# Kernel tuning notes

Measured on AMD Instinct MI355X. Metric: run time of the kernel, lower is better.

The kernel has to match this reference:

```python
import jax, jax.numpy as jnp
import numpy as np

N_NODES = 81920
N_EDGES = 1310720
NODES_PER_GRAPH = 320
N_GRAPHS = N_NODES // NODES_PER_GRAPH  # 256
IN_DIM = 64
HID = 64
OUT = 64


def setup_inputs() -> dict:
    key = jax.random.key(0)
    ks = jax.random.split(key, 16)
    x = jax.random.normal(ks[0], (N_NODES, IN_DIM), dtype=jnp.float32)
    edge_index = jax.random.randint(ks[1], (2, N_EDGES), 0, N_NODES, dtype=jnp.int32)
    # sorted graph-membership vector: 256 graphs of 320 nodes each
    batch = (jnp.arange(N_NODES, dtype=jnp.int32) // NODES_PER_GRAPH)
    std = 1.0  # module re-inits nn.Linear weights with N(0, 1)
    dims = [(IN_DIM, HID), (HID, HID), (HID, OUT)]
    params = {}
    for i, (di, do) in enumerate(dims):
        params[f"Wl{i}"] = std * jax.random.normal(ks[2 + 3 * i], (di, do), dtype=jnp.float32)
        params[f"bl{i}"] = jnp.zeros((do,), dtype=jnp.float32)
        params[f"Wr{i}"] = std * jax.random.normal(ks[3 + 3 * i], (di, do), dtype=jnp.float32)
    return dict(x=x, edge_index=edge_index, batch=batch, **params)


def _sage_conv(x, src, dst, Wl, bl, Wr):
    # PyG SAGEConv (aggr='mean', root_weight=True):
    #   out = lin_l(mean_{j in N(i)} x_j) + lin_r(x_i)
    msg = x[src]                                              # [E, d] gather
    agg = jax.ops.segment_sum(msg, dst, num_segments=N_NODES)  # [N, d] scatter-add
    cnt = jax.ops.segment_sum(jnp.ones((src.shape[0],), x.dtype), dst,
                              num_segments=N_NODES)
    agg = agg / jnp.maximum(cnt, 1.0)[:, None]                # mean aggregation
    return agg @ Wl + bl + x @ Wr


def reference(x, edge_index, batch, Wl0, bl0, Wr0, Wl1, bl1, Wr1, Wl2, bl2, Wr2):
    src, dst = edge_index[0], edge_index[1]
    layers = [(Wl0, bl0, Wr0), (Wl1, bl1, Wr1), (Wl2, bl2, Wr2)]
    h = x
    for i, (Wl, bl, Wr) in enumerate(layers):
        h = _sage_conv(h, src, dst, Wl, bl, Wr)
        if i < len(layers) - 1:
            h = jax.nn.relu(h)
            # F.dropout is identity in eval mode (training=False)
    # unbatch + take node 0 of every graph: first index where batch == g
    first_idx = jnp.searchsorted(batch, jnp.arange(N_GRAPHS, dtype=batch.dtype))
    return h[first_idx]  # [N_GRAPHS, OUT]
```

## Files before the change

### kernel.cpp

```cpp
#include <hip/hip_runtime.h>

#define N_NODES 81920
#define N_EDGES 1310720
#define NG 256
#define D 64
#define TM 64
#define SA 65
#define SB 33
#define SC 36
#define NB 320
#define NBLK 1280
#define BMW 2560
#define HCHUNK 4096
#define EPT 16
#define CAP0 1280
#define CAP1 256
#define CAP2 64

typedef __attribute__((ext_vector_type(2))) short sbf2;

__device__ __forceinline__ bool tb(const unsigned* bm, int i) {
    return (bm[i >> 5] >> (i & 31)) & 1u;
}
__device__ __forceinline__ unsigned bf16rne(float f) {
    unsigned u = __float_as_uint(f);
    return (u + 0x7fffu + ((u >> 16) & 1u)) >> 16;
}
__device__ __forceinline__ float bfl(unsigned u) { return __uint_as_float(u << 16); }
__device__ __forceinline__ float bfh(unsigned u) { return __uint_as_float(u & 0xffff0000u); }


__global__ __launch_bounds__(256) void init_ws(float4* __restrict__ aggb4,
                                               unsigned* __restrict__ bms,
                                               int* __restrict__ indeg,
                                               int* __restrict__ n01,
                                               int* __restrict__ cur0,
                                               int* __restrict__ curS,
                                               int* __restrict__ cur1,
                                               int* __restrict__ cur2,
                                               const float2* __restrict__ x2,
                                               unsigned* __restrict__ xb) {
    int t = blockIdx.x * 256 + threadIdx.x;
    float4 z = make_float4(0.f, 0.f, 0.f, 0.f);
    aggb4[t] = z;
    aggb4[t + NBLK * 256] = z;
    if (t < 3 * BMW) bms[t] = 0u;
    if (t < N_NODES) indeg[t] = 0;
    if (t < 2) n01[t] = 0;
    if (t < NBLK) {
        cur0[t] = t * CAP0;
        curS[t] = t * CAP0;
        cur1[t] = t * CAP1;
        cur2[t] = t * CAP2;
    }
    #pragma unroll
    for (int i = 0; i < 8; ++i) {
        int idx = i * (NBLK * 256) + t;
        float2 v = x2[idx];
        xb[idx] = bf16rne(v.x) | (bf16rne(v.y) << 16);
    }
}


__global__ void ff_mark(const int* __restrict__ batch, int* __restrict__ fidx,
                        unsigned* __restrict__ bm2, unsigned* __restrict__ bm1,
                        float* __restrict__ aggf) {
    int i = blockIdx.x * 256 + threadIdx.x;
    int b = batch[i];
    if (i == 0 || batch[i - 1] != b) {
        fidx[b] = i;
        unsigned bit = 1u << (i & 31);
        atomicOr(&bm2[i >> 5], bit);
        atomicOr(&bm1[i >> 5], bit);
        float4* r = (float4*)&aggf[i * D];
        #pragma unroll
        for (int j = 0; j < 16; ++j) r[j] = make_float4(0.f, 0.f, 0.f, 0.f);
    }
}

__global__ void mark_srcs_bm(const int* __restrict__ src, const int* __restrict__ dst,
                             const unsigned* __restrict__ bmD, unsigned* __restrict__ bmS,
                             const unsigned* __restrict__ orsrc) {
    if (orsrc && blockIdx.x == 0) {
        for (int w = threadIdx.x; w < BMW; w += 256)
            if (orsrc[w]) atomicOr(&bmS[w], orsrc[w]);
    }
    int e = blockIdx.x * 256 + threadIdx.x;
    if (e < N_EDGES && tb(bmD, dst[e])) {
        int s = src[e];
        atomicOr(&bmS[s >> 5], 1u << (s & 31));
    }
}


__global__ __launch_bounds__(256) void build_staged(
    const int* __restrict__ src, const int* __restrict__ dst,
    const unsigned* __restrict__ bm0, const unsigned* __restrict__ bm1,
    const unsigned* __restrict__ bm2,
    int* __restrict__ cur0, int* __restrict__ curS,
    int* __restrict__ cur1, int* __restrict__ cur2,
    int* __restrict__ esp0, int* __restrict__ espS,
    int* __restrict__ esp1, int* __restrict__ esp2,
    int* __restrict__ list1, int* __restrict__ n1)
{
    __shared__ int hd[NBLK];
    __shared__ int hs[NBLK];
    __shared__ int bd[NBLK];
    __shared__ int bs[NBLK];
    const int tid = threadIdx.x;
    const int e0  = blockIdx.x * HCHUNK;

    for (int i = tid; i < NBLK; i += 256) { hd[i] = 0; hs[i] = 0; }

    {
        int i = blockIdx.x * 256 + tid;
        int lane = tid & 63;
        bool p1 = tb(bm1, i);
        unsigned long long b1 = __ballot(p1);
        int lt = __popcll(b1 & ((1ull << lane) - 1));
        int base = 0;
        if (lane == 0 && b1) base = atomicAdd(n1, __popcll(b1));
        base = __shfl(base, 0);
        if (p1) list1[base + lt] = i;
    }
    __syncthreads();

    int pk_r[EPT];
    int md_r[EPT];
    int ms_r[EPT];

    #pragma unroll
    for (int j = 0; j < EPT; ++j) {
        int e = e0 + j * 256 + tid;
        int d = dst[e];
        md_r[j] = -1;
        if (tb(bm0, d)) {
            int s  = src[e];
            int db = d >> 6;
            int sb = s >> 6;
            pk_r[j] = (s << 6) | (d & 63);
            md_r[j] = db | (atomicAdd(&hd[db], 1) << 11);
            ms_r[j] = sb | (atomicAdd(&hs[sb], 1) << 11);
            if (tb(bm1, d)) {
                int pk = (d << 6) | (s & 63);
                int p1 = atomicAdd(&cur1[sb], 1);
                if (p1 < sb * CAP1 + CAP1) esp1[p1] = pk;
                if (tb(bm2, d)) {
                    int p2 = atomicAdd(&cur2[sb], 1);
                    if (p2 < sb * CAP2 + CAP2) esp2[p2] = pk;
                }
            }
        }
    }
    __syncthreads();

    for (int i = tid; i < NBLK; i += 256) {
        int cd = hd[i];
        bd[i] = cd ? atomicAdd(&cur0[i], cd) : 0;
        int cs = hs[i];
        bs[i] = cs ? atomicAdd(&curS[i], cs) : 0;
    }
    __syncthreads();

    #pragma unroll
    for (int j = 0; j < EPT; ++j) {
        int md = md_r[j];
        if (md >= 0) {
            int db = md & 2047;
            int sb = ms_r[j] & 2047;
            int posd = bd[db] + (md >> 11);
            int poss = bs[sb] + (ms_r[j] >> 11);
            if (posd < db * CAP0 + CAP0 && poss < sb * CAP0 + CAP0) {
                esp0[posd] = pk_r[j];
                espS[poss] = (posd << 6) | ((pk_r[j] >> 6) & 63);
            }
        }
    }
}


__global__ __launch_bounds__(256) void build_push(const int* __restrict__ src,
                                                  const int* __restrict__ dst,
                                                  const unsigned* __restrict__ bm0,
                                                  const unsigned* __restrict__ bm1,
                                                  const unsigned* __restrict__ bm2,
                                                  int* __restrict__ cur0,
                                                  int* __restrict__ cur1,
                                                  int* __restrict__ cur2,
                                                  int* __restrict__ esp0,
                                                  int* __restrict__ esp1,
                                                  int* __restrict__ esp2,
                                                  int* __restrict__ indeg,
                                                  int* __restrict__ list1,
                                                  int* __restrict__ n1) {
    __shared__ int h0[NBLK];
    __shared__ int b0[NBLK];
    const int tid = threadIdx.x;
    const int e0  = blockIdx.x * HCHUNK;

    for (int i = tid; i < NBLK; i += 256) h0[i] = 0;

    {
        int i = blockIdx.x * 256 + tid;
        int lane = tid & 63;
        bool p1 = tb(bm1, i);
        unsigned long long b1 = __ballot(p1);
        int lt = __popcll(b1 & ((1ull << lane) - 1));
        int base = 0;
        if (lane == 0 && b1) base = atomicAdd(n1, __popcll(b1));
        base = __shfl(base, 0);
        if (p1) list1[base + lt] = i;
    }
    __syncthreads();

    int pk_r[EPT];
    int sb_r[EPT];
    int rk_r[EPT];

    #pragma unroll
    for (int j = 0; j < EPT; ++j) {
        int e = e0 + j * 256 + tid;
        int d = dst[e];
        sb_r[j] = -1;
        if (tb(bm0, d)) {
            int s  = src[e];
            int sb = s >> 6;
            int pk = (d << 6) | (s & 63);
            pk_r[j] = pk;
            sb_r[j] = sb;
            rk_r[j] = atomicAdd(&h0[sb], 1);
            atomicAdd(&indeg[d], 1);
            if (tb(bm1, d)) {
                int p1 = atomicAdd(&cur1[sb], 1);
                if (p1 < sb * CAP1 + CAP1) esp1[p1] = pk;
                if (tb(bm2, d)) {
                    int p2 = atomicAdd(&cur2[sb], 1);
                    if (p2 < sb * CAP2 + CAP2) esp2[p2] = pk;
                }
            }
        }
    }
    __syncthreads();

    for (int i = tid; i < NBLK; i += 256) {
        int c = h0[i];
        b0[i] = c ? atomicAdd(&cur0[i], c) : 0;
    }
    __syncthreads();

    #pragma unroll
    for (int j = 0; j < EPT; ++j) {
        int sb = sb_r[j];
        if (sb >= 0) {
            int pos = b0[sb] + rk_r[j];
            if (pos < sb * CAP0 + CAP0) esp0[pos] = pk_r[j];
        }
    }
}


__global__ __launch_bounds__(256, 8) void sage_stage_l0(
    const unsigned* __restrict__ xb, const int* __restrict__ curS,
    const int* __restrict__ espS, uint4* __restrict__ stage)
{
    __shared__ unsigned Rs[TM * SC];

    const int tid  = threadIdx.x;
    const int base = blockIdx.x * TM;
    const int lane = tid & 63;
    const int w    = tid >> 6;
    const int g    = lane >> 3;
    const int l3   = lane & 7;

    const int e0 = blockIdx.x * CAP0;
    const int e1 = min(curS[blockIdx.x], e0 + CAP0);
    if (e0 == e1) return;

    for (int idx = tid; idx < TM * 32; idx += 256) {
        int m = idx >> 5, k = idx & 31;
        Rs[m * SC + k] = xb[(base << 5) + idx];
    }
    __syncthreads();

    const int chunk = ((e1 - e0) + 3) >> 2;
    int e = e0 + w * chunk;
    const int ee = min(e + chunk, e1);

    for (; e + 64 <= ee; e += 64) {
        int pv = espS[e + lane];
        #pragma unroll
        for (int u = 0; u < 8; ++u) {
            int p = __shfl(pv, (u << 3) + g);
            uint4 v = *(const uint4*)&Rs[(p & 63) * SC + (l3 << 2)];
            stage[((p >> 6) << 3) + l3] = v;
        }
    }
    for (; e < ee; ++e) {
        int p = espS[e];
        if (lane < 8) {
            uint4 v = *(const uint4*)&Rs[(p & 63) * SC + (lane << 2)];
            stage[((p >> 6) << 3) + lane] = v;
        }
    }
}


__global__ __launch_bounds__(256, 4) void sage_reduce_l0(
    const unsigned* __restrict__ xb, const int* __restrict__ cur0,
    const int* __restrict__ esp0, const uint4* __restrict__ stage,
    int* __restrict__ indeg, float* __restrict__ hout,
    const float* __restrict__ Wl, const float* __restrict__ bl,
    const float* __restrict__ Wr)
{
    __shared__ float As[TM * SA];
    __shared__ float Xs[TM * SA];
    __shared__ float invs[TM];

    const int tid  = threadIdx.x;
    const int base = blockIdx.x * TM;
    const int lane = tid & 63;
    const int w    = tid >> 6;
    const int g    = lane >> 3;
    const int l3   = lane & 7;

    for (int idx = tid; idx < TM * SA; idx += 256) As[idx] = 0.f;
    for (int idx = tid; idx < TM * 32; idx += 256) {
        int m = idx >> 5, k2 = (idx & 31) << 1;
        unsigned xw = xb[(base << 5) + idx];
        Xs[m * SA + k2]     = bfl(xw);
        Xs[m * SA + k2 + 1] = bfh(xw);
    }
    __syncthreads();

    const int e0 = blockIdx.x * CAP0;
    const int e1 = min(cur0[blockIdx.x], e0 + CAP0);

    const int chunk = ((e1 - e0) + 3) >> 2;
    int e = e0 + w * chunk;
    const int ee = min(e + chunk, e1);

    for (; e + 64 <= ee; e += 64) {
        int pv = esp0[e + lane];
        #pragma unroll
        for (int u = 0; u < 8; ++u) {
            int ei = (u << 3) + g;
            int p  = __shfl(pv, ei);
            uint4 v = stage[((e + ei) << 3) + l3];
            int dl = p & 63;
            float* row = &As[dl * SA + (l3 << 3)];
            atomicAdd(&row[0], bfl(v.x));
            atomicAdd(&row[1], bfh(v.x));
            atomicAdd(&row[2], bfl(v.y));
            atomicAdd(&row[3], bfh(v.y));
            atomicAdd(&row[4], bfl(v.z));
            atomicAdd(&row[5], bfh(v.z));
            atomicAdd(&row[6], bfl(v.w));
            atomicAdd(&row[7], bfh(v.w));
            if (l3 == 0) atomicAdd(&As[dl * SA + 64], 1.0f);
        }
    }
    for (; e < ee; ++e) {
        int p = esp0[e];
        if (lane < 8) {
            uint4 v = stage[(e << 3) + lane];
            int dl = p & 63;
            float* row = &As[dl * SA + (lane << 3)];
            atomicAdd(&row[0], bfl(v.x));
            atomicAdd(&row[1], bfh(v.x));
            atomicAdd(&row[2], bfl(v.y));
            atomicAdd(&row[3], bfh(v.y));
            atomicAdd(&row[4], bfl(v.z));
            atomicAdd(&row[5], bfh(v.z));
            atomicAdd(&row[6], bfl(v.w));
            atomicAdd(&row[7], bfh(v.w));
            if (lane == 0) atomicAdd(&As[dl * SA + 64], 1.0f);
        }
    }
    __syncthreads();

    if (tid < TM) {
        int cn = (int)As[tid * SA + 64];
        indeg[base + tid] = cn;
        invs[tid] = 1.0f / (float)max(cn, 1);
    }
    __syncthreads();

    const int j0 = (tid & 7) << 3;
    const int m2 = (tid >> 3) << 1;
    const float iv0 = invs[m2];
    const float iv1 = invs[m2 + 1];
    float o[2][8];
    {
        float4 ba = *(const float4*)&bl[j0];
        float4 bb = *(const float4*)&bl[j0 + 4];
        #pragma unroll
        for (int mi = 0; mi < 2; ++mi) {
            o[mi][0] = ba.x; o[mi][1] = ba.y; o[mi][2] = ba.z; o[mi][3] = ba.w;
            o[mi][4] = bb.x; o[mi][5] = bb.y; o[mi][6] = bb.z; o[mi][7] = bb.w;
        }
    }
    #pragma unroll 8
    for (int k = 0; k < D; ++k) {
        float a0 = As[m2 * SA + k] * iv0;
        float a1 = As[(m2 + 1) * SA + k] * iv1;
        float x0 = Xs[m2 * SA + k];
        float x1 = Xs[(m2 + 1) * SA + k];
        float4 wl0 = *(const float4*)&Wl[(k << 6) + j0];
        float4 wl1 = *(const float4*)&Wl[(k << 6) + j0 + 4];
        float4 wr0 = *(const float4*)&Wr[(k << 6) + j0];
        float4 wr1 = *(const float4*)&Wr[(k << 6) + j0 + 4];
        o[0][0] += a0 * wl0.x + x0 * wr0.x;  o[1][0] += a1 * wl0.x + x1 * wr0.x;
        o[0][1] += a0 * wl0.y + x0 * wr0.y;  o[1][1] += a1 * wl0.y + x1 * wr0.y;
        o[0][2] += a0 * wl0.z + x0 * wr0.z;  o[1][2] += a1 * wl0.z + x1 * wr0.z;
        o[0][3] += a0 * wl0.w + x0 * wr0.w;  o[1][3] += a1 * wl0.w + x1 * wr0.w;
        o[0][4] += a0 * wl1.x + x0 * wr1.x;  o[1][4] += a1 * wl1.x + x1 * wr1.x;
        o[0][5] += a0 * wl1.y + x0 * wr1.y;  o[1][5] += a1 * wl1.y + x1 * wr1.y;
        o[0][6] += a0 * wl1.z + x0 * wr1.z;  o[1][6] += a1 * wl1.z + x1 * wr1.z;
        o[0][7] += a0 * wl1.w + x0 * wr1.w;  o[1][7] += a1 * wl1.w + x1 * wr1.w;
    }
    #pragma unroll
    for (int mi = 0; mi < 2; ++mi) {
        float4 r0 = make_float4(fmaxf(o[mi][0], 0.f), fmaxf(o[mi][1], 0.f),
                                fmaxf(o[mi][2], 0.f), fmaxf(o[mi][3], 0.f));
        float4 r1 = make_float4(fmaxf(o[mi][4], 0.f), fmaxf(o[mi][5], 0.f),
                                fmaxf(o[mi][6], 0.f), fmaxf(o[mi][7], 0.f));
        *(float4*)&hout[(base + m2 + mi) * D + j0]     = r0;
        *(float4*)&hout[(base + m2 + mi) * D + j0 + 4] = r1;
    }
}


__global__ __launch_bounds__(256, 8) void sage_push_bf_pre(
    const unsigned* __restrict__ xb, const int* __restrict__ cur,
    const int* __restrict__ esp, unsigned* __restrict__ aggb, int cap)
{
    __shared__ unsigned Rs[TM * SB];

    const int tid  = threadIdx.x;
    const int base = blockIdx.x * TM;
    const int lane = tid & 63;
    const int w    = tid >> 6;
    const int l5   = lane & 31;
    const int hi   = lane >> 5;

    const int e0 = blockIdx.x * cap;
    const int e1 = min(cur[blockIdx.x], e0 + cap);
    if (e0 == e1) return;

    for (int idx = tid; idx < TM * 32; idx += 256) {
        int m = idx >> 5, k = idx & 31;
        Rs[m * SB + k] = xb[(base << 5) + idx];
    }
    __syncthreads();

    const int chunk = ((e1 - e0) + 3) >> 2;
    int e = e0 + w * chunk;
    const int ee = min(e + chunk, e1);

    for (; e + 64 <= ee; e += 64) {
        int pv = esp[e + lane];
        #pragma unroll
        for (int u = 0; u < 32; ++u) {
            int p = __shfl(pv, (u << 1) + hi);
            unsigned v = Rs[(p & 63) * SB + l5];
            __builtin_amdgcn_global_atomic_fadd_v2bf16(
                (sbf2*)&aggb[((p >> 6) << 5) + l5], *(sbf2*)&v);
        }
    }
    for (; e < ee; ++e) {
        int p = esp[e];
        if (!hi) {
            unsigned v = Rs[(p & 63) * SB + l5];
            __builtin_amdgcn_global_atomic_fadd_v2bf16(
                (sbf2*)&aggb[((p >> 6) << 5) + l5], *(sbf2*)&v);
        }
    }
}


__global__ __launch_bounds__(256, 8) void sage_push_bf(
    const float* __restrict__ hin, const int* __restrict__ cur,
    const int* __restrict__ esp, unsigned* __restrict__ aggb, int cap)
{
    __shared__ unsigned Rs[TM * SB];

    const int tid  = threadIdx.x;
    const int base = blockIdx.x * TM;
    const int lane = tid & 63;
    const int w    = tid >> 6;
    const int l5   = lane & 31;
    const int hi   = lane >> 5;

    const int e0 = blockIdx.x * cap;
    const int e1 = min(cur[blockIdx.x], e0 + cap);
    if (e0 == e1) return;

    for (int idx = tid; idx < TM * 32; idx += 256) {
        int m = idx >> 5, k = idx & 31;
        float2 v = *(const float2*)&hin[((base + m) << 6) + (k << 1)];
        Rs[m * SB + k] = bf16rne(v.x) | (bf16rne(v.y) << 16);
    }
    __syncthreads();

    const int chunk = ((e1 - e0) + 3) >> 2;
    int e = e0 + w * chunk;
    const int ee = min(e + chunk, e1);

    for (; e + 64 <= ee; e += 64) {
        int pv = esp[e + lane];
        #pragma unroll
        for (int u = 0; u < 32; ++u) {
            int p = __shfl(pv, (u << 1) + hi);
            unsigned v = Rs[(p & 63) * SB + l5];
            __builtin_amdgcn_global_atomic_fadd_v2bf16(
                (sbf2*)&aggb[((p >> 6) << 5) + l5], *(sbf2*)&v);
        }
    }
    for (; e < ee; ++e) {
        int p = esp[e];
        if (!hi) {
            unsigned v = Rs[(p & 63) * SB + l5];
            __builtin_amdgcn_global_atomic_fadd_v2bf16(
                (sbf2*)&aggb[((p >> 6) << 5) + l5], *(sbf2*)&v);
        }
    }
}


__global__ __launch_bounds__(256, 8) void sage_push_f32(
    const float* __restrict__ hin, const int* __restrict__ cur,
    const int* __restrict__ esp, float* __restrict__ agg, int cap)
{
    __shared__ float Rs[TM * SA];

    const int tid  = threadIdx.x;
    const int base = blockIdx.x * TM;
    const int lane = tid & 63;
    const int w    = tid >> 6;

    const int e0 = blockIdx.x * cap;
    const int e1 = min(cur[blockIdx.x], e0 + cap);
    if (e0 == e1) return;

    for (int idx = tid; idx < TM * D; idx += 256) {
        int m = idx >> 6, k = idx & 63;
        Rs[m * SA + k] = hin[(base << 6) + idx];
    }
    __syncthreads();

    const int chunk = ((e1 - e0) + 3) >> 2;
    int e = e0 + w * chunk;
    const int ee = min(e + chunk, e1);

    for (; e < ee; ++e) {
        int p = esp[e];
        atomicAdd(&agg[(p & 0x7fffffc0) + lane], Rs[(p & 63) * SA + lane]);
    }
}


__global__ __launch_bounds__(256, 4) void sage_finish_dense(
    const unsigned* __restrict__ xb, unsigned* __restrict__ aggb,
    const int* __restrict__ indeg, float* __restrict__ hout,
    const float* __restrict__ Wl, const float* __restrict__ bl,
    const float* __restrict__ Wr)
{
    __shared__ float As[TM * SA];
    __shared__ float Xs[TM * SA];
    __shared__ float invs[TM];

    const int tid  = threadIdx.x;
    const int base = blockIdx.x * TM;

    if (tid < TM) invs[tid] = 1.0f / (float)max(indeg[base + tid], 1);
    for (int idx = tid; idx < TM * 32; idx += 256) {
        int m = idx >> 5, k2 = (idx & 31) << 1;
        unsigned v = aggb[(base << 5) + idx];
        As[m * SA + k2]     = bfl(v);
        As[m * SA + k2 + 1] = bfh(v);
        aggb[(base << 5) + idx] = 0u;
        unsigned xw = xb[(base << 5) + idx];
        Xs[m * SA + k2]     = bfl(xw);
        Xs[m * SA + k2 + 1] = bfh(xw);
    }
    __syncthreads();
    for (int idx = tid; idx < TM * D; idx += 256) {
        int m = idx >> 6, k = idx & 63;
        As[m * SA + k] *= invs[m];
    }
    __syncthreads();

    const int j0 = (tid & 15) << 2;
    const int m0 = (tid >> 4) << 2;
    float o[4][4];
    float4 b4 = *(const float4*)&bl[j0];
    #pragma unroll
    for (int mi = 0; mi < 4; ++mi) {
        o[mi][0] = b4.x; o[mi][1] = b4.y; o[mi][2] = b4.z; o[mi][3] = b4.w;
    }
    #pragma unroll 8
    for (int k = 0; k < D; ++k) {
        float4 wl = *(const float4*)&Wl[(k << 6) + j0];
        float4 wr = *(const float4*)&Wr[(k << 6) + j0];
        #pragma unroll
        for (int mi = 0; mi < 4; ++mi) {
            float a = As[(m0 + mi) * SA + k];
            float x = Xs[(m0 + mi) * SA + k];
            o[mi][0] += a * wl.x + x * wr.x;
            o[mi][1] += a * wl.y + x * wr.y;
            o[mi][2] += a * wl.z + x * wr.z;
            o[mi][3] += a * wl.w + x * wr.w;
        }
    }
    #pragma unroll
    for (int mi = 0; mi < 4; ++mi) {
        float4 r = make_float4(fmaxf(o[mi][0], 0.f), fmaxf(o[mi][1], 0.f),
                               fmaxf(o[mi][2], 0.f), fmaxf(o[mi][3], 0.f));
        *(float4*)&hout[(base + m0 + mi) * D + j0] = r;
    }
}


__global__ __launch_bounds__(256, 4) void sage_finish_sel(
    const float* __restrict__ hin, unsigned* __restrict__ aggb,
    const int* __restrict__ indeg, const int* __restrict__ list,
    const int* __restrict__ pcount, float* __restrict__ hout,
    const float* __restrict__ Wl, const float* __restrict__ bl,
    const float* __restrict__ Wr)
{
    __shared__ float As[TM * SA];
    __shared__ float Xs[TM * SA];
    __shared__ float invs[TM];
    __shared__ int   nid[TM];

    const int cntv = *pcount;
    const int base = blockIdx.x * TM;
    if (base >= cntv) return;

    const int tid = threadIdx.x;
    if (tid < TM) {
        int n = (base + tid < cntv) ? list[base + tid] : -1;
        nid[tid]  = n;
        invs[tid] = (n >= 0) ? 1.0f / (float)max(indeg[n], 1) : 0.f;
    }
    __syncthreads();
    for (int idx = tid; idx < TM * 32; idx += 256) {
        int m = idx >> 5, k2 = idx & 31;
        int n = nid[m];
        if (n >= 0) {
            unsigned v = aggb[(n << 5) + k2];
            As[m * SA + (k2 << 1)]     = bfl(v) * invs[m];
            As[m * SA + (k2 << 1) + 1] = bfh(v) * invs[m];
        } else {
            As[m * SA + (k2 << 1)]     = 0.f;
            As[m * SA + (k2 << 1) + 1] = 0.f;
        }
    }
    for (int idx = tid; idx < TM * D; idx += 256) {
        int m = idx >> 6, k = idx & 63;
        int n = nid[m];
        Xs[m * SA + k] = (n >= 0) ? hin[n * D + k] : 0.f;
    }
    __syncthreads();

    const int j0 = (tid & 15) << 2;
    const int m0 = (tid >> 4) << 2;
    float o[4][4];
    float4 b4 = *(const float4*)&bl[j0];
    #pragma unroll
    for (int mi = 0; mi < 4; ++mi) {
        o[mi][0] = b4.x; o[mi][1] = b4.y; o[mi][2] = b4.z; o[mi][3] = b4.w;
    }
    #pragma unroll 8
    for (int k = 0; k < D; ++k) {
        float4 wl = *(const float4*)&Wl[(k << 6) + j0];
        float4 wr = *(const float4*)&Wr[(k << 6) + j0];
        #pragma unroll
        for (int mi = 0; mi < 4; ++mi) {
            float a = As[(m0 + mi) * SA + k];
            float x = Xs[(m0 + mi) * SA + k];
            o[mi][0] += a * wl.x + x * wr.x;
            o[mi][1] += a * wl.y + x * wr.y;
            o[mi][2] += a * wl.z + x * wr.z;
            o[mi][3] += a * wl.w + x * wr.w;
        }
    }
    #pragma unroll
    for (int mi = 0; mi < 4; ++mi) {
        int n = nid[m0 + mi];
        if (n >= 0) {
            float4 r = make_float4(fmaxf(o[mi][0], 0.f), fmaxf(o[mi][1], 0.f),
                                   fmaxf(o[mi][2], 0.f), fmaxf(o[mi][3], 0.f));
            *(float4*)&hout[n * D + j0] = r;
        }
    }
}


__global__ __launch_bounds__(256, 3) void final_gemm_sel(
    const float* __restrict__ hin, const float* __restrict__ agg,
    const int* __restrict__ indeg, const int* __restrict__ fidx,
    const float* __restrict__ Wl, const float* __restrict__ bl,
    const float* __restrict__ Wr, float* __restrict__ out)
{
    __shared__ float As[TM * SA];
    __shared__ float Xs[TM * SA];
    __shared__ int   nid[TM];
    __shared__ float invs[TM];

    const int tid  = threadIdx.x;
    const int base = blockIdx.x * TM;

    if (tid < TM) {
        int n = fidx[base + tid];
        nid[tid]  = n;
        invs[tid] = 1.0f / (float)max(indeg[n], 1);
    }
    __syncthreads();
    for (int idx = tid; idx < TM * D; idx += 256) {
        int m = idx >> 6, k = idx & 63;
        int n = nid[m];
        As[m * SA + k] = agg[n * D + k] * invs[m];
        Xs[m * SA + k] = hin[n * D + k];
    }
    __syncthreads();

    const int j0 = (tid & 15) << 2;
    const int m0 = (tid >> 4) << 2;
    float o[4][4];
    float4 b4 = *(const float4*)&bl[j0];
    #pragma unroll
    for (int mi = 0; mi < 4; ++mi) {
        o[mi][0] = b4.x; o[mi][1] = b4.y; o[mi][2] = b4.z; o[mi][3] = b4.w;
    }
    #pragma unroll 8
    for (int k = 0; k < D; ++k) {
        float4 wl = *(const float4*)&Wl[(k << 6) + j0];
        float4 wr = *(const float4*)&Wr[(k << 6) + j0];
        #pragma unroll
        for (int mi = 0; mi < 4; ++mi) {
            float a = As[(m0 + mi) * SA + k];
            float x = Xs[(m0 + mi) * SA + k];
            o[mi][0] += a * wl.x + x * wr.x;
            o[mi][1] += a * wl.y + x * wr.y;
            o[mi][2] += a * wl.z + x * wr.z;
            o[mi][3] += a * wl.w + x * wr.w;
        }
    }
    #pragma unroll
    for (int mi = 0; mi < 4; ++mi) {
        float4 r = make_float4(o[mi][0], o[mi][1], o[mi][2], o[mi][3]);
        *(float4*)&out[(base + m0 + mi) * D + j0] = r;
    }
}


extern "C" void kernel_launch(void* const* d_in, const int* in_sizes, int n_in,
                              void* d_out, int out_size, void* d_ws, size_t ws_size,
                              hipStream_t stream)
{
    const float* x     = (const float*)d_in[0];
    const int*   ei    = (const int*)d_in[1];
    const int*   batch = (const int*)d_in[2];
    const float* Wl0 = (const float*)d_in[3];
    const float* bl0 = (const float*)d_in[4];
    const float* Wr0 = (const float*)d_in[5];
    const float* Wl1 = (const float*)d_in[6];
    const float* bl1 = (const float*)d_in[7];
    const float* Wr1 = (const float*)d_in[8];
    const float* Wl2 = (const float*)d_in[9];
    const float* bl2 = (const float*)d_in[10];
    const float* Wr2 = (const float*)d_in[11];
    float* out = (float*)d_out;

    const int* src = ei;
    const int* dst = ei + N_EDGES;

    char* ws = (char*)d_ws;
    size_t off = 0;
    auto alloc = [&](size_t bytes) -> void* {
        void* p = ws + off;
        off = (off + bytes + 255) & ~(size_t)255;
        return p;
    };
    int*      cur0  = (int*)alloc(NBLK * sizeof(int));
    int*      curS  = (int*)alloc(NBLK * sizeof(int));
    int*      cur1  = (int*)alloc(NBLK * sizeof(int));
    int*      cur2  = (int*)alloc(NBLK * sizeof(int));
    int*      fidx  = (int*)alloc(NG * sizeof(int));
    int*      list1 = (int*)alloc(N_NODES * sizeof(int));
    int*      esp0  = (int*)alloc((size_t)NBLK * CAP0 * sizeof(int));
    int*      espS  = (int*)alloc((size_t)NBLK * CAP0 * sizeof(int));
    int*      esp1  = (int*)alloc((size_t)NBLK * CAP1 * sizeof(int));
    int*      esp2  = (int*)alloc((size_t)NBLK * CAP2 * sizeof(int));
    unsigned* aggb  = (unsigned*)alloc((size_t)N_NODES * 32 * sizeof(unsigned));
    float*    aggf  = (float*)alloc((size_t)N_NODES * D * sizeof(float));
    float*    h1    = (float*)alloc((size_t)N_NODES * D * sizeof(float));
    float*    h2    = (float*)alloc((size_t)N_NODES * D * sizeof(float));
    unsigned* bms   = (unsigned*)alloc((size_t)3 * BMW * sizeof(unsigned));
    int*      indeg = (int*)alloc(N_NODES * sizeof(int));
    int*      n01   = (int*)alloc(64 * sizeof(int));
    uint4*    stage = (uint4*)alloc((size_t)NBLK * CAP0 * 128);
    const bool staged = (off <= ws_size);
    unsigned* bm0 = bms;
    unsigned* bm1 = bms + BMW;
    unsigned* bm2 = bms + 2 * BMW;
    int* n1 = n01 + 1;
    unsigned* xb = (unsigned*)h2;
    (void)in_sizes; (void)n_in; (void)out_size;

    const int EB = (N_EDGES + 255) / 256;

    init_ws<<<NBLK, 256, 0, stream>>>((float4*)aggb, bms, indeg, n01,
                                      cur0, curS, cur1, cur2, (const float2*)x, xb);
    ff_mark<<<NB, 256, 0, stream>>>(batch, fidx, bm2, bm1, aggf);
    mark_srcs_bm<<<EB, 256, 0, stream>>>(src, dst, bm2, bm1, (const unsigned*)nullptr);
    mark_srcs_bm<<<EB, 256, 0, stream>>>(src, dst, bm1, bm0, bm1);

    if (staged) {
        build_staged<<<NB, 256, 0, stream>>>(src, dst, bm0, bm1, bm2,
                                             cur0, curS, cur1, cur2,
                                             esp0, espS, esp1, esp2, list1, n1);
        sage_stage_l0 <<<NBLK, 256, 0, stream>>>(xb, curS, espS, stage);
        sage_reduce_l0<<<NBLK, 256, 0, stream>>>(xb, cur0, esp0, stage,
                                                 indeg, h1, Wl0, bl0, Wr0);
    } else {
        build_push<<<NB, 256, 0, stream>>>(src, dst, bm0, bm1, bm2, cur0, cur1, cur2,
                                           esp0, esp1, esp2, indeg, list1, n1);
        sage_push_bf_pre <<<NBLK, 256, 0, stream>>>(xb, cur0, esp0, aggb, CAP0);
        sage_finish_dense<<<NBLK, 256, 0, stream>>>(xb, aggb, indeg, h1, Wl0, bl0, Wr0);
    }

    sage_push_bf     <<<NBLK, 256, 0, stream>>>(h1, cur1, esp1, aggb, CAP1);
    sage_finish_sel  <<<NBLK, 256, 0, stream>>>(h1, aggb, indeg, list1, n1,
                                                h2, Wl1, bl1, Wr1);
    sage_push_f32    <<<NBLK, 256, 0, stream>>>(h2, cur2, esp2, aggf, CAP2);
    final_gemm_sel   <<<NG / TM, 256, 0, stream>>>(h2, aggf, indeg, fidx, Wl2, bl2, Wr2, out);
}
```

Before: 416.8 us.

## Alias stage buffer onto aggf and process layer-0 staging in destination-block groups

The layer-0 stage buffer now overlays the aggf region, so the staged path is enabled when the workspace can hold at least 320 destination blocks of stage data. When space is short, it loops over groups of destination blocks: each pass reruns the full stage kernel but writes only the entries in range, then reduces that group. aggf rows for the first node of each graph are re-zeroed afterwards, since the stage writes overwrite them. The goal is to use the staged path instead of the push fallback on smaller workspaces, at the cost of repeated stage passes and extra launches.

```diff
diff --git a/kernel.cpp b/kernel.cpp
--- a/kernel.cpp
+++ b/kernel.cpp
@@ -78,6 +78,13 @@
     }
 }
 
+__global__ void zero_aggf(float* __restrict__ aggf, const int* __restrict__ fidx) {
+    int n = fidx[threadIdx.x];
+    float4* r = (float4*)&aggf[n * D];
+    #pragma unroll
+    for (int j = 0; j < 16; ++j) r[j] = make_float4(0.f, 0.f, 0.f, 0.f);
+}
+
 __global__ void mark_srcs_bm(const int* __restrict__ src, const int* __restrict__ dst,
                              const unsigned* __restrict__ bmD, unsigned* __restrict__ bmS,
                              const unsigned* __restrict__ orsrc) {
@@ -261,7 +268,8 @@
 
 __global__ __launch_bounds__(256, 8) void sage_stage_l0(
     const unsigned* __restrict__ xb, const int* __restrict__ curS,
-    const int* __restrict__ espS, uint4* __restrict__ stage)
+    const int* __restrict__ espS, uint4* __restrict__ stage,
+    int plo, int phi)
 {
     __shared__ unsigned Rs[TM * SC];
 
@@ -291,15 +299,19 @@
         #pragma unroll
         for (int u = 0; u < 8; ++u) {
             int p = __shfl(pv, (u << 3) + g);
-            uint4 v = *(const uint4*)&Rs[(p & 63) * SC + (l3 << 2)];
-            stage[((p >> 6) << 3) + l3] = v;
+            int posd = p >> 6;
+            if (posd >= plo && posd < phi) {
+                uint4 v = *(const uint4*)&Rs[(p & 63) * SC + (l3 << 2)];
+                stage[((posd - plo) << 3) + l3] = v;
+            }
         }
     }
     for (; e < ee; ++e) {
         int p = espS[e];
-        if (lane < 8) {
+        int posd = p >> 6;
+        if (lane < 8 && posd >= plo && posd < phi) {
             uint4 v = *(const uint4*)&Rs[(p & 63) * SC + (lane << 2)];
-            stage[((p >> 6) << 3) + lane] = v;
+            stage[((posd - plo) << 3) + lane] = v;
         }
     }
 }
@@ -308,7 +320,7 @@
 __global__ __launch_bounds__(256, 4) void sage_reduce_l0(
     const unsigned* __restrict__ xb, const int* __restrict__ cur0,
     const int* __restrict__ esp0, const uint4* __restrict__ stage,
-    int* __restrict__ indeg, float* __restrict__ hout,
+    int dblk0, int* __restrict__ indeg, float* __restrict__ hout,
     const float* __restrict__ Wl, const float* __restrict__ bl,
     const float* __restrict__ Wr)
 {
@@ -317,7 +329,9 @@
     __shared__ float invs[TM];
 
     const int tid  = threadIdx.x;
-    const int base = blockIdx.x * TM;
+    const int db   = blockIdx.x + dblk0;
+    const int base = db * TM;
+    const int plo  = dblk0 * CAP0;
     const int lane = tid & 63;
     const int w    = tid >> 6;
     const int g    = lane >> 3;
@@ -332,8 +346,8 @@
     }
     __syncthreads();
 
-    const int e0 = blockIdx.x * CAP0;
-    const int e1 = min(cur0[blockIdx.x], e0 + CAP0);
+    const int e0 = db * CAP0;
+    const int e1 = min(cur0[db], e0 + CAP0);
 
     const int chunk = ((e1 - e0) + 3) >> 2;
     int e = e0 + w * chunk;
@@ -345,7 +359,7 @@
         for (int u = 0; u < 8; ++u) {
             int ei = (u << 3) + g;
             int p  = __shfl(pv, ei);
-            uint4 v = stage[((e + ei) << 3) + l3];
+            uint4 v = stage[((e + ei - plo) << 3) + l3];
             int dl = p & 63;
             float* row = &As[dl * SA + (l3 << 3)];
             atomicAdd(&row[0], bfl(v.x));
@@ -362,7 +376,7 @@
     for (; e < ee; ++e) {
         int p = esp0[e];
         if (lane < 8) {
-            uint4 v = stage[(e << 3) + lane];
+            uint4 v = stage[((e - plo) << 3) + lane];
             int dl = p & 63;
             float* row = &As[dl * SA + (lane << 3)];
             atomicAdd(&row[0], bfl(v.x));
@@ -794,14 +808,18 @@
     int*      esp1  = (int*)alloc((size_t)NBLK * CAP1 * sizeof(int));
     int*      esp2  = (int*)alloc((size_t)NBLK * CAP2 * sizeof(int));
     unsigned* aggb  = (unsigned*)alloc((size_t)N_NODES * 32 * sizeof(unsigned));
-    float*    aggf  = (float*)alloc((size_t)N_NODES * D * sizeof(float));
     float*    h1    = (float*)alloc((size_t)N_NODES * D * sizeof(float));
     float*    h2    = (float*)alloc((size_t)N_NODES * D * sizeof(float));
     unsigned* bms   = (unsigned*)alloc((size_t)3 * BMW * sizeof(unsigned));
     int*      indeg = (int*)alloc(N_NODES * sizeof(int));
     int*      n01   = (int*)alloc(64 * sizeof(int));
-    uint4*    stage = (uint4*)alloc((size_t)NBLK * CAP0 * 128);
-    const bool staged = (off <= ws_size);
+    float*    aggf  = (float*)alloc((size_t)N_NODES * D * sizeof(float));
+    uint4*    stage = (uint4*)aggf;
+    size_t stage_avail = (ws_size > (off - (size_t)N_NODES * D * sizeof(float)))
+                       ? ws_size - (off - (size_t)N_NODES * D * sizeof(float)) : 0;
+    int bpg = (int)((stage_avail / ((size_t)CAP0 * 128)) < (size_t)NBLK
+                    ? (stage_avail / ((size_t)CAP0 * 128)) : (size_t)NBLK);
+    const bool staged = (bpg >= 320);
     unsigned* bm0 = bms;
     unsigned* bm1 = bms + BMW;
     unsigned* bm2 = bms + 2 * BMW;
@@ -821,9 +839,17 @@
         build_staged<<<NB, 256, 0, stream>>>(src, dst, bm0, bm1, bm2,
                                              cur0, curS, cur1, cur2,
                                              esp0, espS, esp1, esp2, list1, n1);
-        sage_stage_l0 <<<NBLK, 256, 0, stream>>>(xb, curS, espS, stage);
-        sage_reduce_l0<<<NBLK, 256, 0, stream>>>(xb, cur0, esp0, stage,
-                                                 indeg, h1, Wl0, bl0, Wr0);
+        const int G = (NBLK + bpg - 1) / bpg;
+        for (int g = 0; g < G; ++g) {
+            int dlo = g * bpg;
+            int dhi = (dlo + bpg < NBLK) ? dlo + bpg : NBLK;
+            sage_stage_l0 <<<NBLK, 256, 0, stream>>>(xb, curS, espS, stage,
+                                                     dlo * CAP0, dhi * CAP0);
+            sage_reduce_l0<<<dhi - dlo, 256, 0, stream>>>(xb, cur0, esp0, stage,
+                                                          dlo, indeg, h1,
+                                                          Wl0, bl0, Wr0);
+        }
+        zero_aggf<<<1, 256, 0, stream>>>(aggf, fidx);
     } else {
         build_push<<<NB, 256, 0, stream>>>(src, dst, bm0, bm1, bm2, cur0, cur1, cur2,
                                            esp0, esp1, esp2, indeg, list1, n1);
```

Measured after the change: 678.2 us. 1.63x slower.
